# Kernel optimization log

Hardware: AMD Instinct MI355X
Metric: run time of the kernel (lower is better)

Reference implementation:

```python
import jax, jax.numpy as jnp
import numpy as np

NEG_SLOPE = 0.2


def gat_conv(x, src, dst, W, a_src, a_dst, b, heads, ch, n_nodes):
    # x: [N, F_in] -> h: [N, H, C]
    h = (x @ W).reshape(n_nodes, heads, ch)
    alpha_src = (h * a_src).sum(-1)  # [N, H]
    alpha_dst = (h * a_dst).sum(-1)  # [N, H]
    e = jax.nn.leaky_relu(alpha_src[src] + alpha_dst[dst], NEG_SLOPE)  # [E, H]
    # segment softmax over destination neighborhoods (every node has a self-loop)
    m = jax.ops.segment_max(e, dst, num_segments=n_nodes)
    e = jnp.exp(e - m[dst])
    s = jax.ops.segment_sum(e, dst, num_segments=n_nodes)
    alpha = e / s[dst]  # [E, H]
    out = jax.ops.segment_sum(h[src] * alpha[:, :, None], dst, num_segments=n_nodes)
    return out.reshape(n_nodes, heads * ch) + b


def setup_inputs() -> dict:
    key = jax.random.key(0)
    ks = jax.random.split(key, 12)
    N, E = 50000, 800000
    F_in, HID, H, OUT = 128, 64, 2, 64
    x = jax.random.normal(ks[0], (N, F_in), dtype=jnp.float32)
    edge_index = jax.random.randint(ks[1], (2, E), 0, N, dtype=jnp.int64)
    s1 = 1.0 / np.sqrt(F_in)
    s2 = 1.0 / np.sqrt(H * HID)
    return {
        "x": x,
        "edge_index": edge_index,
        "W1": jax.random.normal(ks[2], (F_in, H * HID), dtype=jnp.float32) * s1,
        "att_src1": jax.random.normal(ks[3], (H, HID), dtype=jnp.float32) * s1,
        "att_dst1": jax.random.normal(ks[4], (H, HID), dtype=jnp.float32) * s1,
        "b1": jnp.zeros((H * HID,), dtype=jnp.float32),
        "W2": jax.random.normal(ks[5], (H * HID, OUT), dtype=jnp.float32) * s2,
        "att_src2": jax.random.normal(ks[6], (1, OUT), dtype=jnp.float32) * s2,
        "att_dst2": jax.random.normal(ks[7], (1, OUT), dtype=jnp.float32) * s2,
        "b2": jnp.zeros((OUT,), dtype=jnp.float32),
    }


def reference(x, edge_index, W1, att_src1, att_dst1, b1, W2, att_src2, att_dst2, b2):
    N = x.shape[0]
    # PyG GATConv adds self-loops by default
    loops = jnp.arange(N, dtype=edge_index.dtype)
    src = jnp.concatenate([edge_index[0], loops])
    dst = jnp.concatenate([edge_index[1], loops])
    h = gat_conv(x, src, dst, W1, att_src1, att_dst1, b1, 2, 64, N)
    h = jax.nn.relu(h)
    out = gat_conv(h, src, dst, W2, att_src2, att_dst2, b2, 1, 64, N)
    return jax.nn.sigmoid(out)
```

## Files before the change

kernel.cpp:

```cpp
#include <hip/hip_runtime.h>
#include <math.h>

#define N_NODES 50000
#define N_EDGES 800000
#define E_TOT   (N_EDGES + N_NODES)
#define NEG_SLOPE 0.2f
#define NB_BKT  ((N_NODES + 255) / 256)
#define BKT_CAP 5632
#define P1_CHUNK 4096
#define NB_P1   ((E_TOT + P1_CHUNK - 1) / P1_CHUNK)
#define NB_G1   ((N_NODES + 127) / 128)

typedef short bf16x8 __attribute__((ext_vector_type(8)));
typedef float f32x4 __attribute__((ext_vector_type(4)));

static __device__ __forceinline__ float lrelu(float v) {
    return v > 0.0f ? v : NEG_SLOPE * v;
}

static __device__ __forceinline__ unsigned short f2bf(float f) {
    unsigned b = __float_as_uint(f);
    return (unsigned short)((b + 0x7fffu + ((b >> 16) & 1u)) >> 16);
}

static __device__ __forceinline__ float bflo(unsigned u) { return __uint_as_float(u << 16); }
static __device__ __forceinline__ float bfhi(unsigned u) { return __uint_as_float(u & 0xffff0000u); }

static __device__ __forceinline__ int swz(int row, int k) {
    return row * 128 + ((((k >> 3) ^ (row & 15)) << 3) | (k & 7));
}
static __device__ __forceinline__ int swz64(int row, int c) {
    return row * 64 + ((((c >> 3) ^ (row & 7)) << 3) | (c & 7));
}

__global__ __launch_bounds__(256, 2) void fusedA_kernel(const float* __restrict__ x,
                                                        const float* __restrict__ W,
                                                        const float* __restrict__ a_src,
                                                        const float* __restrict__ a_dst,
                                                        unsigned short* __restrict__ h1b,
                                                        float* __restrict__ as_out,
                                                        float* __restrict__ ad_out,
                                                        const int* __restrict__ ei,
                                                        int* __restrict__ bktcnt,
                                                        uint2* __restrict__ pairs) {
    __shared__ __align__(16) unsigned char smem[65536];
    int tid = threadIdx.x;

    if (blockIdx.x >= NB_G1) {
        int* cnt  = (int*)smem;
        int* base = (int*)(smem + 1024);
        for (int i = tid; i < NB_BKT; i += 256) cnt[i] = 0;
        __syncthreads();
        int cbase = (blockIdx.x - NB_G1) * P1_CHUNK;
        for (int i = tid; i < P1_CHUNK; i += 256) {
            int e = cbase + i;
            if (e >= E_TOT) break;
            int d = (e < N_EDGES) ? ei[N_EDGES + e] : (e - N_EDGES);
            atomicAdd(&cnt[d >> 8], 1);
        }
        __syncthreads();
        for (int i = tid; i < NB_BKT; i += 256) {
            int c = cnt[i];
            base[i] = c ? (BKT_CAP * i + atomicAdd(&bktcnt[i], c)) : 0;
            cnt[i] = 0;
        }
        __syncthreads();
        for (int i = tid; i < P1_CHUNK; i += 256) {
            int e = cbase + i;
            if (e >= E_TOT) break;
            int s, d;
            if (e < N_EDGES) { s = ei[e]; d = ei[N_EDGES + e]; }
            else { s = d = e - N_EDGES; }
            int bk = d >> 8;
            int p = base[bk] + atomicAdd(&cnt[bk], 1);
            pairs[p] = make_uint2((unsigned)s, (unsigned)d);
        }
        return;
    }

    unsigned short* xs = (unsigned short*)smem;
    unsigned short* wt = (unsigned short*)(smem + 32768);
    int r0 = blockIdx.x * 128;

    {
        int n = tid & 127;
        int c0 = (tid >> 7) * 8;
        for (int c = c0; c < c0 + 8; ++c) {
            int kb = c * 8;
            ushort4 lo, hi;
            lo.x = f2bf(W[(kb + 0) * 128 + n]);
            lo.y = f2bf(W[(kb + 1) * 128 + n]);
            lo.z = f2bf(W[(kb + 2) * 128 + n]);
            lo.w = f2bf(W[(kb + 3) * 128 + n]);
            hi.x = f2bf(W[(kb + 4) * 128 + n]);
            hi.y = f2bf(W[(kb + 5) * 128 + n]);
            hi.z = f2bf(W[(kb + 6) * 128 + n]);
            hi.w = f2bf(W[(kb + 7) * 128 + n]);
            int a = swz(n, kb);
            *(ushort4*)&wt[a] = lo;
            *(ushort4*)&wt[a + 4] = hi;
        }
    }
    {
        const int maxe = N_NODES * 128 - 4;
#pragma unroll
        for (int i = 0; i < 16384; i += 1024) {
            int e = i + tid * 4;
            int ge = r0 * 128 + e;
            if (ge > maxe) ge = maxe;
            float4 v = *(const float4*)&x[ge];
            ushort4 p;
            p.x = f2bf(v.x); p.y = f2bf(v.y); p.z = f2bf(v.z); p.w = f2bf(v.w);
            *(ushort4*)&xs[swz(e >> 7, e & 127)] = p;
        }
    }
    __syncthreads();

    int wv = tid >> 6, lane = tid & 63, lm = lane & 15, quad = lane >> 4;
    f32x4 acc[2][8];
#pragma unroll
    for (int m = 0; m < 2; ++m)
#pragma unroll
        for (int n = 0; n < 8; ++n) acc[m][n] = (f32x4){0.f, 0.f, 0.f, 0.f};

#pragma unroll
    for (int kc = 0; kc < 4; ++kc) {
        int kb = kc * 32 + quad * 8;
        bf16x8 a0 = *(bf16x8*)&xs[swz(wv * 32 + lm, kb)];
        bf16x8 a1 = *(bf16x8*)&xs[swz(wv * 32 + 16 + lm, kb)];
#pragma unroll
        for (int nt = 0; nt < 8; ++nt) {
            bf16x8 b = *(bf16x8*)&wt[swz(nt * 16 + lm, kb)];
            acc[0][nt] = __builtin_amdgcn_mfma_f32_16x16x32_bf16(a0, b, acc[0][nt], 0, 0, 0);
            acc[1][nt] = __builtin_amdgcn_mfma_f32_16x16x32_bf16(a1, b, acc[1][nt], 0, 0, 0);
        }
    }

    float asv[8], adv[8];
#pragma unroll
    for (int nt = 0; nt < 8; ++nt) {
        asv[nt] = a_src[nt * 16 + lm];
        adv[nt] = a_dst[nt * 16 + lm];
    }
#pragma unroll
    for (int mt = 0; mt < 2; ++mt) {
#pragma unroll
        for (int r = 0; r < 4; ++r) {
            float s0 = 0.f, s1 = 0.f, d0 = 0.f, d1 = 0.f;
#pragma unroll
            for (int nt = 0; nt < 4; ++nt) {
                s0 += acc[mt][nt][r] * asv[nt];
                d0 += acc[mt][nt][r] * adv[nt];
            }
#pragma unroll
            for (int nt = 4; nt < 8; ++nt) {
                s1 += acc[mt][nt][r] * asv[nt];
                d1 += acc[mt][nt][r] * adv[nt];
            }
#pragma unroll
            for (int m = 1; m < 16; m <<= 1) {
                s0 += __shfl_xor(s0, m, 64);
                s1 += __shfl_xor(s1, m, 64);
                d0 += __shfl_xor(d0, m, 64);
                d1 += __shfl_xor(d1, m, 64);
            }
            if (lm == 0) {
                int gr = r0 + wv * 32 + mt * 16 + quad * 4 + r;
                if (gr < N_NODES) {
                    as_out[gr * 2 + 0] = s0;
                    as_out[gr * 2 + 1] = s1;
                    ad_out[gr * 2 + 0] = d0;
                    ad_out[gr * 2 + 1] = d1;
                }
            }
        }
    }

    __syncthreads();
#pragma unroll
    for (int mt = 0; mt < 2; ++mt) {
#pragma unroll
        for (int nt = 0; nt < 8; ++nt) {
#pragma unroll
            for (int r = 0; r < 4; ++r) {
                int lrow = wv * 32 + mt * 16 + quad * 4 + r;
                xs[swz(lrow, nt * 16 + lm)] = f2bf(acc[mt][nt][r]);
            }
        }
    }
    __syncthreads();
    {
        int lrow = tid >> 1;
        int cb = (tid & 1) * 64;
        int gr = r0 + lrow;
        if (gr < N_NODES) {
            unsigned short* dst = h1b + (size_t)gr * 128 + cb;
#pragma unroll
            for (int c = 0; c < 8; ++c)
                *(uint4*)(dst + c * 8) = *(uint4*)&xs[swz(lrow, cb + c * 8)];
        }
    }
}

__global__ void scatterP2_kernel(const uint2* __restrict__ pairs, const int* __restrict__ bktcnt,
                                 int* __restrict__ offsets, int* __restrict__ deg,
                                 int* __restrict__ csr_src) {
    __shared__ int cnt[256];
    __shared__ int scn[256];
    int t = threadIdx.x;
    int b = blockIdx.x;
    int node0 = b << 8;
    int pbase = b * BKT_CAP;
    int cntE = bktcnt[b];
    cnt[t] = 0;
    __syncthreads();
    for (int j = t; j < cntE; j += 256)
        atomicAdd(&cnt[pairs[pbase + j].y - node0], 1);
    __syncthreads();
    int v = cnt[t];
    scn[t] = v;
    __syncthreads();
#pragma unroll
    for (int off = 1; off < 256; off <<= 1) {
        int u = (t >= off) ? scn[t - off] : 0;
        __syncthreads();
        scn[t] += u;
        __syncthreads();
    }
    int start = pbase + scn[t] - v;
    if (node0 + t < N_NODES) {
        offsets[node0 + t] = start;
        deg[node0 + t] = v;
    }
    cnt[t] = start;
    __syncthreads();
    for (int j = t; j < cntE; j += 256) {
        uint2 pr = pairs[pbase + j];
        int p = atomicAdd(&cnt[pr.y - node0], 1);
        csr_src[p] = (int)pr.x;
    }
}

__global__ __launch_bounds__(256, 2) void gemm2_kernel(const unsigned short* __restrict__ xb,
                                                       const float* __restrict__ W,
                                                       const float* __restrict__ a_src,
                                                       const float* __restrict__ a_dst,
                                                       unsigned short* __restrict__ h2b,
                                                       float* __restrict__ as_out,
                                                       float* __restrict__ ad_out) {
    __shared__ unsigned short xs[128 * 128];
    __shared__ unsigned short wt[64 * 128];
    int tid = threadIdx.x;
    int r0 = blockIdx.x * 128;

    {
        int n = tid & 63;
        int c0 = (tid >> 6) * 4;
        for (int c = c0; c < c0 + 4; ++c) {
            int kb = c * 8;
            ushort4 lo, hi;
            lo.x = f2bf(W[(kb + 0) * 64 + n]);
            lo.y = f2bf(W[(kb + 1) * 64 + n]);
            lo.z = f2bf(W[(kb + 2) * 64 + n]);
            lo.w = f2bf(W[(kb + 3) * 64 + n]);
            hi.x = f2bf(W[(kb + 4) * 64 + n]);
            hi.y = f2bf(W[(kb + 5) * 64 + n]);
            hi.z = f2bf(W[(kb + 6) * 64 + n]);
            hi.w = f2bf(W[(kb + 7) * 64 + n]);
            int a = swz(n, kb);
            *(ushort4*)&wt[a] = lo;
            *(ushort4*)&wt[a + 4] = hi;
        }
    }
    {
        const int maxe = N_NODES * 128 - 8;
#pragma unroll
        for (int i = 0; i < 16384; i += 2048) {
            int e = i + tid * 8;
            int ge = r0 * 128 + e;
            if (ge > maxe) ge = maxe;
            uint4 v = *(const uint4*)&xb[ge];
            *(uint4*)&xs[swz(e >> 7, e & 127)] = v;
        }
    }
    __syncthreads();

    int wv = tid >> 6, lane = tid & 63, lm = lane & 15, quad = lane >> 4;
    f32x4 acc[2][4];
#pragma unroll
    for (int m = 0; m < 2; ++m)
#pragma unroll
        for (int n = 0; n < 4; ++n) acc[m][n] = (f32x4){0.f, 0.f, 0.f, 0.f};

#pragma unroll
    for (int kc = 0; kc < 4; ++kc) {
        int kb = kc * 32 + quad * 8;
        bf16x8 a0 = *(bf16x8*)&xs[swz(wv * 32 + lm, kb)];
        bf16x8 a1 = *(bf16x8*)&xs[swz(wv * 32 + 16 + lm, kb)];
#pragma unroll
        for (int nt = 0; nt < 4; ++nt) {
            bf16x8 b = *(bf16x8*)&wt[swz(nt * 16 + lm, kb)];
            acc[0][nt] = __builtin_amdgcn_mfma_f32_16x16x32_bf16(a0, b, acc[0][nt], 0, 0, 0);
            acc[1][nt] = __builtin_amdgcn_mfma_f32_16x16x32_bf16(a1, b, acc[1][nt], 0, 0, 0);
        }
    }

    float asv[4], adv[4];
#pragma unroll
    for (int nt = 0; nt < 4; ++nt) {
        asv[nt] = a_src[nt * 16 + lm];
        adv[nt] = a_dst[nt * 16 + lm];
    }
#pragma unroll
    for (int mt = 0; mt < 2; ++mt) {
#pragma unroll
        for (int r = 0; r < 4; ++r) {
            float s0 = 0.f, d0 = 0.f;
#pragma unroll
            for (int nt = 0; nt < 4; ++nt) {
                s0 += acc[mt][nt][r] * asv[nt];
                d0 += acc[mt][nt][r] * adv[nt];
            }
#pragma unroll
            for (int m = 1; m < 16; m <<= 1) {
                s0 += __shfl_xor(s0, m, 64);
                d0 += __shfl_xor(d0, m, 64);
            }
            if (lm == 0) {
                int gr = r0 + wv * 32 + mt * 16 + quad * 4 + r;
                if (gr < N_NODES) {
                    as_out[gr] = s0;
                    ad_out[gr] = d0;
                }
            }
        }
    }

    __syncthreads();
#pragma unroll
    for (int mt = 0; mt < 2; ++mt) {
#pragma unroll
        for (int nt = 0; nt < 4; ++nt) {
#pragma unroll
            for (int r = 0; r < 4; ++r) {
                int lrow = wv * 32 + mt * 16 + quad * 4 + r;
                wt[swz64(lrow, nt * 16 + lm)] = f2bf(acc[mt][nt][r]);
            }
        }
    }
    __syncthreads();
    {
        int lrow = tid >> 1;
        int cb = (tid & 1) * 32;
        int gr = r0 + lrow;
        if (gr < N_NODES) {
            unsigned short* dst = h2b + (size_t)gr * 64 + cb;
#pragma unroll
            for (int c = 0; c < 4; ++c)
                *(uint4*)(dst + c * 8) = *(uint4*)&wt[swz64(lrow, cb + c * 8)];
        }
    }
}

__global__ void agg1_kernel(const unsigned short* __restrict__ h1b,
                            const float* __restrict__ as1,
                            const float* __restrict__ ad1, const float* __restrict__ b1,
                            const int* __restrict__ offsets, const int* __restrict__ deg,
                            const int* __restrict__ csr_src,
                            unsigned short* __restrict__ out1b) {
    int wid = (blockIdx.x * blockDim.x + threadIdx.x) >> 6;
    if (wid >= N_NODES) return;
    int lane = threadIdx.x & 63;
    int cl = lane & 31;
    int half = lane >> 5;
    bool head1 = (cl >= 16);
    float da0 = ad1[wid * 2 + 0], da1 = ad1[wid * 2 + 1];
    int jb = offsets[wid], je = jb + deg[wid];
    float a0 = 0.f, a1 = 0.f, a2 = 0.f, a3 = 0.f;
    float psum0 = 0.f, psum1 = 0.f;

    for (int chunk = jb; chunk < je; chunk += 64) {
        int j = chunk + lane;
        int s = 0; float w0 = 0.f, w1 = 0.f;
        if (j < je) {
            s = csr_src[j];
            float2 av = *(const float2*)&as1[s * 2];
            w0 = __expf(lrelu(av.x + da0));
            w1 = __expf(lrelu(av.y + da1));
        }
        psum0 += w0; psum1 += w1;
        int cnt = je - chunk; if (cnt > 64) cnt = 64;
        for (int k = 0; k < cnt; k += 8) {
            int k0 = k + half, k1 = k + 2 + half, k2 = k + 4 + half, k3 = k + 6 + half;
            int ss0 = __shfl(s, k0, 64);
            int ss1 = __shfl(s, k1, 64);
            int ss2 = __shfl(s, k2, 64);
            int ss3 = __shfl(s, k3, 64);
            uint2 u0 = ((const uint2*)(h1b + (size_t)ss0 * 128))[cl];
            uint2 u1 = ((const uint2*)(h1b + (size_t)ss1 * 128))[cl];
            uint2 u2 = ((const uint2*)(h1b + (size_t)ss2 * 128))[cl];
            uint2 u3 = ((const uint2*)(h1b + (size_t)ss3 * 128))[cl];
            float p0 = __shfl(w0, k0, 64), q0 = __shfl(w1, k0, 64);
            float p1 = __shfl(w0, k1, 64), q1 = __shfl(w1, k1, 64);
            float p2 = __shfl(w0, k2, 64), q2 = __shfl(w1, k2, 64);
            float p3 = __shfl(w0, k3, 64), q3 = __shfl(w1, k3, 64);
            float bw0 = head1 ? q0 : p0;
            float bw1 = head1 ? q1 : p1;
            float bw2 = head1 ? q2 : p2;
            float bw3 = head1 ? q3 : p3;
            a0 += bw0 * bflo(u0.x); a1 += bw0 * bfhi(u0.x); a2 += bw0 * bflo(u0.y); a3 += bw0 * bfhi(u0.y);
            a0 += bw1 * bflo(u1.x); a1 += bw1 * bfhi(u1.x); a2 += bw1 * bflo(u1.y); a3 += bw1 * bfhi(u1.y);
            a0 += bw2 * bflo(u2.x); a1 += bw2 * bfhi(u2.x); a2 += bw2 * bflo(u2.y); a3 += bw2 * bfhi(u2.y);
            a0 += bw3 * bflo(u3.x); a1 += bw3 * bfhi(u3.x); a2 += bw3 * bflo(u3.y); a3 += bw3 * bfhi(u3.y);
        }
    }
#pragma unroll
    for (int m = 1; m < 64; m <<= 1) {
        psum0 += __shfl_xor(psum0, m, 64);
        psum1 += __shfl_xor(psum1, m, 64);
    }
    float o0 = __shfl(a0, cl + 32, 64);
    float o1 = __shfl(a1, cl + 32, 64);
    float o2 = __shfl(a2, cl + 32, 64);
    float o3 = __shfl(a3, cl + 32, 64);
    if (lane < 32) {
        float inv = 1.f / (head1 ? psum1 : psum0);
        float4 bv = *(const float4*)&b1[cl * 4];
        float v0 = (a0 + o0) * inv + bv.x;
        float v1 = (a1 + o1) * inv + bv.y;
        float v2 = (a2 + o2) * inv + bv.z;
        float v3 = (a3 + o3) * inv + bv.w;
        v0 = v0 > 0.f ? v0 : 0.f;
        v1 = v1 > 0.f ? v1 : 0.f;
        v2 = v2 > 0.f ? v2 : 0.f;
        v3 = v3 > 0.f ? v3 : 0.f;
        ushort4 p;
        p.x = f2bf(v0); p.y = f2bf(v1); p.z = f2bf(v2); p.w = f2bf(v3);
        *(ushort4*)&out1b[(size_t)wid * 128 + cl * 4] = p;
    }
}

__global__ void agg2_kernel(const unsigned short* __restrict__ h2b,
                            const float* __restrict__ as2,
                            const float* __restrict__ ad2, const float* __restrict__ b2,
                            const int* __restrict__ offsets, const int* __restrict__ deg,
                            const int* __restrict__ csr_src,
                            float* __restrict__ out) {
    int wid = (blockIdx.x * blockDim.x + threadIdx.x) >> 6;
    if (wid >= N_NODES) return;
    int lane = threadIdx.x & 63;
    int cl = lane & 31;
    int half = lane >> 5;
    float da = ad2[wid];
    int jb = offsets[wid], je = jb + deg[wid];
    float acc0 = 0.f, acc1 = 0.f, psum = 0.f;

    for (int chunk = jb; chunk < je; chunk += 64) {
        int j = chunk + lane;
        int s = 0; float w = 0.f;
        if (j < je) {
            s = csr_src[j];
            w = __expf(lrelu(as2[s] + da));
        }
        psum += w;
        int cnt = je - chunk; if (cnt > 64) cnt = 64;
        for (int k = 0; k < cnt; k += 8) {
            int k0 = k + half, k1 = k + 2 + half, k2 = k + 4 + half, k3 = k + 6 + half;
            int ss0 = __shfl(s, k0, 64);
            int ss1 = __shfl(s, k1, 64);
            int ss2 = __shfl(s, k2, 64);
            int ss3 = __shfl(s, k3, 64);
            unsigned u0 = ((const unsigned*)(h2b + (size_t)ss0 * 64))[cl];
            unsigned u1 = ((const unsigned*)(h2b + (size_t)ss1 * 64))[cl];
            unsigned u2 = ((const unsigned*)(h2b + (size_t)ss2 * 64))[cl];
            unsigned u3 = ((const unsigned*)(h2b + (size_t)ss3 * 64))[cl];
            float bw0 = __shfl(w, k0, 64);
            float bw1 = __shfl(w, k1, 64);
            float bw2 = __shfl(w, k2, 64);
            float bw3 = __shfl(w, k3, 64);
            acc0 += bw0 * bflo(u0); acc1 += bw0 * bfhi(u0);
            acc0 += bw1 * bflo(u1); acc1 += bw1 * bfhi(u1);
            acc0 += bw2 * bflo(u2); acc1 += bw2 * bfhi(u2);
            acc0 += bw3 * bflo(u3); acc1 += bw3 * bfhi(u3);
        }
    }
#pragma unroll
    for (int m = 1; m < 64; m <<= 1) psum += __shfl_xor(psum, m, 64);
    float o0 = __shfl(acc0, cl + 32, 64);
    float o1 = __shfl(acc1, cl + 32, 64);
    if (lane < 32) {
        float inv = 1.f / psum;
        float2 bv = *(const float2*)&b2[cl * 2];
        float v0 = (acc0 + o0) * inv + bv.x;
        float v1 = (acc1 + o1) * inv + bv.y;
        v0 = 1.f / (1.f + __expf(-v0));
        v1 = 1.f / (1.f + __expf(-v1));
        *(float2*)&out[(size_t)wid * 64 + cl * 2] = make_float2(v0, v1);
    }
}

extern "C" void kernel_launch(void* const* d_in, const int* in_sizes, int n_in,
                              void* d_out, int out_size, void* d_ws, size_t ws_size,
                              hipStream_t stream) {
    const float* x     = (const float*)d_in[0];
    const int*   ei    = (const int*)d_in[1];
    const float* W1    = (const float*)d_in[2];
    const float* asrc1 = (const float*)d_in[3];
    const float* adst1 = (const float*)d_in[4];
    const float* b1    = (const float*)d_in[5];
    const float* W2    = (const float*)d_in[6];
    const float* asrc2 = (const float*)d_in[7];
    const float* adst2 = (const float*)d_in[8];
    const float* b2    = (const float*)d_in[9];
    float* out = (float*)d_out;

    float* ws = (float*)d_ws;
    size_t off = 0;
    float* as1  = ws + off; off += (size_t)N_NODES * 2;
    float* ad1  = ws + off; off += (size_t)N_NODES * 2;
    float* as2  = ws + off; off += (size_t)N_NODES;
    float* ad2  = ws + off; off += (size_t)N_NODES;
    unsigned short* h1b   = (unsigned short*)(ws + off); off += (size_t)N_NODES * 64;
    unsigned short* out1b = (unsigned short*)(ws + off); off += (size_t)N_NODES * 64;
    unsigned short* h2b   = (unsigned short*)(ws + off); off += (size_t)N_NODES * 32;
    int* offsets = (int*)(ws + off);
    int* deg     = offsets + N_NODES;
    int* csr_src = deg + N_NODES;
    int* bktcnt  = csr_src + NB_BKT * BKT_CAP;
    uint2* pairs = (uint2*)((((size_t)(bktcnt + NB_BKT)) + 7) & ~(size_t)7);

    hipMemsetAsync(bktcnt, 0, NB_BKT * sizeof(int), stream);

    fusedA_kernel<<<NB_G1 + NB_P1, 256, 0, stream>>>(x, W1, asrc1, adst1, h1b, as1, ad1,
                                                     ei, bktcnt, pairs);
    scatterP2_kernel<<<NB_BKT, 256, 0, stream>>>(pairs, bktcnt, offsets, deg, csr_src);
    agg1_kernel<<<(N_NODES * 64 + 255) / 256, 256, 0, stream>>>(h1b, as1, ad1, b1, offsets, deg, csr_src, out1b);
    gemm2_kernel<<<NB_G1, 256, 0, stream>>>(out1b, W2, asrc2, adst2, h2b, as2, ad2);
    agg2_kernel<<<(N_NODES * 64 + 255) / 256, 256, 0, stream>>>(h2b, as2, ad2, b2, offsets, deg, csr_src, out);
}
```

Baseline: 194.0 us.

## Fuse CSR scatter into layer-1 aggregation and store 16-bit source indices

Removes the separate scatter kernel: the layer-1 aggregation kernel now builds its bucket's CSR slice in shared memory and aggregates directly from it. Buckets shrink to 128 nodes and use 1024-thread blocks. Source indices are stored as unsigned short to halve index traffic in agg2. The cost is far fewer, larger blocks, which may reduce occupancy or balance in the gather-heavy aggregation.

```diff
diff --git a/kernel.cpp b/kernel.cpp
--- a/kernel.cpp
+++ b/kernel.cpp
@@ -5,8 +5,9 @@
 #define N_EDGES 800000
 #define E_TOT   (N_EDGES + N_NODES)
 #define NEG_SLOPE 0.2f
-#define NB_BKT  ((N_NODES + 255) / 256)
-#define BKT_CAP 5632
+#define NPB      128
+#define NB_BKT  ((N_NODES + NPB - 1) / NPB)
+#define BKT_CAP 3200
 #define P1_CHUNK 4096
 #define NB_P1   ((E_TOT + P1_CHUNK - 1) / P1_CHUNK)
 #define NB_G1   ((N_NODES + 127) / 128)
@@ -48,7 +49,7 @@
 
     if (blockIdx.x >= NB_G1) {
         int* cnt  = (int*)smem;
-        int* base = (int*)(smem + 1024);
+        int* base = (int*)(smem + 2048);
         for (int i = tid; i < NB_BKT; i += 256) cnt[i] = 0;
         __syncthreads();
         int cbase = (blockIdx.x - NB_G1) * P1_CHUNK;
@@ -56,7 +57,7 @@
             int e = cbase + i;
             if (e >= E_TOT) break;
             int d = (e < N_EDGES) ? ei[N_EDGES + e] : (e - N_EDGES);
-            atomicAdd(&cnt[d >> 8], 1);
+            atomicAdd(&cnt[d >> 7], 1);
         }
         __syncthreads();
         for (int i = tid; i < NB_BKT; i += 256) {
@@ -71,7 +72,7 @@
             int s, d;
             if (e < N_EDGES) { s = ei[e]; d = ei[N_EDGES + e]; }
             else { s = d = e - N_EDGES; }
-            int bk = d >> 8;
+            int bk = d >> 7;
             int p = base[bk] + atomicAdd(&cnt[bk], 1);
             pairs[p] = make_uint2((unsigned)s, (unsigned)d);
         }
@@ -202,42 +203,133 @@
     }
 }
 
-__global__ void scatterP2_kernel(const uint2* __restrict__ pairs, const int* __restrict__ bktcnt,
-                                 int* __restrict__ offsets, int* __restrict__ deg,
-                                 int* __restrict__ csr_src) {
-    __shared__ int cnt[256];
-    __shared__ int scn[256];
+__global__ __launch_bounds__(1024) void agg1_kernel(const unsigned short* __restrict__ h1b,
+                                                    const float* __restrict__ as1,
+                                                    const float* __restrict__ ad1,
+                                                    const float* __restrict__ b1,
+                                                    const uint2* __restrict__ pairs,
+                                                    const int* __restrict__ bktcnt,
+                                                    int* __restrict__ offsets,
+                                                    int* __restrict__ deg,
+                                                    unsigned short* __restrict__ csr_us,
+                                                    unsigned short* __restrict__ out1b) {
+    __shared__ unsigned short srcs[BKT_CAP];
+    __shared__ int cntL[NPB];
+    __shared__ int offL[NPB];
     int t = threadIdx.x;
     int b = blockIdx.x;
-    int node0 = b << 8;
+    int node0 = b * NPB;
     int pbase = b * BKT_CAP;
     int cntE = bktcnt[b];
-    cnt[t] = 0;
-    __syncthreads();
-    for (int j = t; j < cntE; j += 256)
-        atomicAdd(&cnt[pairs[pbase + j].y - node0], 1);
-    __syncthreads();
-    int v = cnt[t];
-    scn[t] = v;
-    __syncthreads();
-#pragma unroll
-    for (int off = 1; off < 256; off <<= 1) {
-        int u = (t >= off) ? scn[t - off] : 0;
+
+    if (t < NPB) cntL[t] = 0;
+    __syncthreads();
+    for (int j = t; j < cntE; j += 1024)
+        atomicAdd(&cntL[pairs[pbase + j].y - node0], 1);
+    __syncthreads();
+    int c = (t < NPB) ? cntL[t] : 0;
+    if (t < NPB) offL[t] = c;
+    __syncthreads();
+#pragma unroll
+    for (int off = 1; off < NPB; off <<= 1) {
+        int u = (t >= off && t < NPB) ? offL[t - off] : 0;
         __syncthreads();
-        scn[t] += u;
+        if (t < NPB) offL[t] += u;
         __syncthreads();
     }
-    int start = pbase + scn[t] - v;
-    if (node0 + t < N_NODES) {
-        offsets[node0 + t] = start;
-        deg[node0 + t] = v;
-    }
-    cnt[t] = start;
-    __syncthreads();
-    for (int j = t; j < cntE; j += 256) {
+    int excl = (t < NPB) ? (offL[t] - c) : 0;
+    if (t < NPB) {
+        int node = node0 + t;
+        if (node < N_NODES) {
+            offsets[node] = pbase + excl;
+            deg[node] = c;
+        }
+    }
+    __syncthreads();
+    if (t < NPB) { offL[t] = excl; cntL[t] = excl; }
+    __syncthreads();
+    for (int j = t; j < cntE; j += 1024) {
         uint2 pr = pairs[pbase + j];
-        int p = atomicAdd(&cnt[pr.y - node0], 1);
-        csr_src[p] = (int)pr.x;
+        int p = atomicAdd(&cntL[pr.y - node0], 1);
+        srcs[p] = (unsigned short)pr.x;
+    }
+    __syncthreads();
+    for (int j = t; j < cntE; j += 1024)
+        csr_us[pbase + j] = srcs[j];
+
+    int wv = t >> 6, lane = t & 63;
+    int cl = lane & 31;
+    int half = lane >> 5;
+    bool head1 = (cl >= 16);
+#pragma unroll
+    for (int nt = 0; nt < 8; ++nt) {
+        int nl = wv * 8 + nt;
+        int node = node0 + nl;
+        if (node >= N_NODES) continue;
+        int jb = offL[nl], je = cntL[nl];
+        float da0 = ad1[node * 2 + 0], da1 = ad1[node * 2 + 1];
+        float a0 = 0.f, a1 = 0.f, a2 = 0.f, a3 = 0.f;
+        float psum0 = 0.f, psum1 = 0.f;
+
+        for (int chunk = jb; chunk < je; chunk += 64) {
+            int j = chunk + lane;
+            int s = 0; float w0 = 0.f, w1 = 0.f;
+            if (j < je) {
+                s = (int)srcs[j];
+                float2 av = *(const float2*)&as1[s * 2];
+                w0 = __expf(lrelu(av.x + da0));
+                w1 = __expf(lrelu(av.y + da1));
+            }
+            psum0 += w0; psum1 += w1;
+            int cnt = je - chunk; if (cnt > 64) cnt = 64;
+            for (int k = 0; k < cnt; k += 8) {
+                int k0 = k + half, k1 = k + 2 + half, k2 = k + 4 + half, k3 = k + 6 + half;
+                int ss0 = __shfl(s, k0, 64);
+                int ss1 = __shfl(s, k1, 64);
+                int ss2 = __shfl(s, k2, 64);
+                int ss3 = __shfl(s, k3, 64);
+                uint2 u0 = ((const uint2*)(h1b + (size_t)ss0 * 128))[cl];
+                uint2 u1 = ((const uint2*)(h1b + (size_t)ss1 * 128))[cl];
+                uint2 u2 = ((const uint2*)(h1b + (size_t)ss2 * 128))[cl];
+                uint2 u3 = ((const uint2*)(h1b + (size_t)ss3 * 128))[cl];
+                float p0 = __shfl(w0, k0, 64), q0 = __shfl(w1, k0, 64);
+                float p1 = __shfl(w0, k1, 64), q1 = __shfl(w1, k1, 64);
+                float p2 = __shfl(w0, k2, 64), q2 = __shfl(w1, k2, 64);
+                float p3 = __shfl(w0, k3, 64), q3 = __shfl(w1, k3, 64);
+                float bw0 = head1 ? q0 : p0;
+                float bw1 = head1 ? q1 : p1;
+                float bw2 = head1 ? q2 : p2;
+                float bw3 = head1 ? q3 : p3;
+                a0 += bw0 * bflo(u0.x); a1 += bw0 * bfhi(u0.x); a2 += bw0 * bflo(u0.y); a3 += bw0 * bfhi(u0.y);
+                a0 += bw1 * bflo(u1.x); a1 += bw1 * bfhi(u1.x); a2 += bw1 * bflo(u1.y); a3 += bw1 * bfhi(u1.y);
+                a0 += bw2 * bflo(u2.x); a1 += bw2 * bfhi(u2.x); a2 += bw2 * bflo(u2.y); a3 += bw2 * bfhi(u2.y);
+                a0 += bw3 * bflo(u3.x); a1 += bw3 * bfhi(u3.x); a2 += bw3 * bflo(u3.y); a3 += bw3 * bfhi(u3.y);
+            }
+        }
+#pragma unroll
+        for (int m = 1; m < 64; m <<= 1) {
+            psum0 += __shfl_xor(psum0, m, 64);
+            psum1 += __shfl_xor(psum1, m, 64);
+        }
+        float o0 = __shfl(a0, cl + 32, 64);
+        float o1 = __shfl(a1, cl + 32, 64);
+        float o2 = __shfl(a2, cl + 32, 64);
+        float o3 = __shfl(a3, cl + 32, 64);
+        if (lane < 32) {
+            float inv = 1.f / (head1 ? psum1 : psum0);
+            float4 bv = *(const float4*)&b1[cl * 4];
+            float v0 = (a0 + o0) * inv + bv.x;
+            float v1 = (a1 + o1) * inv + bv.y;
+            float v2 = (a2 + o2) * inv + bv.z;
+            float v3 = (a3 + o3) * inv + bv.w;
+            v0 = v0 > 0.f ? v0 : 0.f;
+            v1 = v1 > 0.f ? v1 : 0.f;
+            v2 = v2 > 0.f ? v2 : 0.f;
+            v3 = v3 > 0.f ? v3 : 0.f;
+            ushort4 p;
+            p.x = f2bf(v0); p.y = f2bf(v1); p.z = f2bf(v2); p.w = f2bf(v3);
+            *(ushort4*)&out1b[(size_t)node * 128 + cl * 4] = p;
+        }
     }
 }
 
@@ -362,89 +454,11 @@
     }
 }
 
-__global__ void agg1_kernel(const unsigned short* __restrict__ h1b,
-                            const float* __restrict__ as1,
-                            const float* __restrict__ ad1, const float* __restrict__ b1,
-                            const int* __restrict__ offsets, const int* __restrict__ deg,
-                            const int* __restrict__ csr_src,
-                            unsigned short* __restrict__ out1b) {
-    int wid = (blockIdx.x * blockDim.x + threadIdx.x) >> 6;
-    if (wid >= N_NODES) return;
-    int lane = threadIdx.x & 63;
-    int cl = lane & 31;
-    int half = lane >> 5;
-    bool head1 = (cl >= 16);
-    float da0 = ad1[wid * 2 + 0], da1 = ad1[wid * 2 + 1];
-    int jb = offsets[wid], je = jb + deg[wid];
-    float a0 = 0.f, a1 = 0.f, a2 = 0.f, a3 = 0.f;
-    float psum0 = 0.f, psum1 = 0.f;
-
-    for (int chunk = jb; chunk < je; chunk += 64) {
-        int j = chunk + lane;
-        int s = 0; float w0 = 0.f, w1 = 0.f;
-        if (j < je) {
-            s = csr_src[j];
-            float2 av = *(const float2*)&as1[s * 2];
-            w0 = __expf(lrelu(av.x + da0));
-            w1 = __expf(lrelu(av.y + da1));
-        }
-        psum0 += w0; psum1 += w1;
-        int cnt = je - chunk; if (cnt > 64) cnt = 64;
-        for (int k = 0; k < cnt; k += 8) {
-            int k0 = k + half, k1 = k + 2 + half, k2 = k + 4 + half, k3 = k + 6 + half;
-            int ss0 = __shfl(s, k0, 64);
-            int ss1 = __shfl(s, k1, 64);
-            int ss2 = __shfl(s, k2, 64);
-            int ss3 = __shfl(s, k3, 64);
-            uint2 u0 = ((const uint2*)(h1b + (size_t)ss0 * 128))[cl];
-            uint2 u1 = ((const uint2*)(h1b + (size_t)ss1 * 128))[cl];
-            uint2 u2 = ((const uint2*)(h1b + (size_t)ss2 * 128))[cl];
-            uint2 u3 = ((const uint2*)(h1b + (size_t)ss3 * 128))[cl];
-            float p0 = __shfl(w0, k0, 64), q0 = __shfl(w1, k0, 64);
-            float p1 = __shfl(w0, k1, 64), q1 = __shfl(w1, k1, 64);
-            float p2 = __shfl(w0, k2, 64), q2 = __shfl(w1, k2, 64);
-            float p3 = __shfl(w0, k3, 64), q3 = __shfl(w1, k3, 64);
-            float bw0 = head1 ? q0 : p0;
-            float bw1 = head1 ? q1 : p1;
-            float bw2 = head1 ? q2 : p2;
-            float bw3 = head1 ? q3 : p3;
-            a0 += bw0 * bflo(u0.x); a1 += bw0 * bfhi(u0.x); a2 += bw0 * bflo(u0.y); a3 += bw0 * bfhi(u0.y);
-            a0 += bw1 * bflo(u1.x); a1 += bw1 * bfhi(u1.x); a2 += bw1 * bflo(u1.y); a3 += bw1 * bfhi(u1.y);
-            a0 += bw2 * bflo(u2.x); a1 += bw2 * bfhi(u2.x); a2 += bw2 * bflo(u2.y); a3 += bw2 * bfhi(u2.y);
-            a0 += bw3 * bflo(u3.x); a1 += bw3 * bfhi(u3.x); a2 += bw3 * bflo(u3.y); a3 += bw3 * bfhi(u3.y);
-        }
-    }
-#pragma unroll
-    for (int m = 1; m < 64; m <<= 1) {
-        psum0 += __shfl_xor(psum0, m, 64);
-        psum1 += __shfl_xor(psum1, m, 64);
-    }
-    float o0 = __shfl(a0, cl + 32, 64);
-    float o1 = __shfl(a1, cl + 32, 64);
-    float o2 = __shfl(a2, cl + 32, 64);
-    float o3 = __shfl(a3, cl + 32, 64);
-    if (lane < 32) {
-        float inv = 1.f / (head1 ? psum1 : psum0);
-        float4 bv = *(const float4*)&b1[cl * 4];
-        float v0 = (a0 + o0) * inv + bv.x;
-        float v1 = (a1 + o1) * inv + bv.y;
-        float v2 = (a2 + o2) * inv + bv.z;
-        float v3 = (a3 + o3) * inv + bv.w;
-        v0 = v0 > 0.f ? v0 : 0.f;
-        v1 = v1 > 0.f ? v1 : 0.f;
-        v2 = v2 > 0.f ? v2 : 0.f;
-        v3 = v3 > 0.f ? v3 : 0.f;
-        ushort4 p;
-        p.x = f2bf(v0); p.y = f2bf(v1); p.z = f2bf(v2); p.w = f2bf(v3);
-        *(ushort4*)&out1b[(size_t)wid * 128 + cl * 4] = p;
-    }
-}
-
 __global__ void agg2_kernel(const unsigned short* __restrict__ h2b,
                             const float* __restrict__ as2,
                             const float* __restrict__ ad2, const float* __restrict__ b2,
                             const int* __restrict__ offsets, const int* __restrict__ deg,
-                            const int* __restrict__ csr_src,
+                            const unsigned short* __restrict__ csr_us,
                             float* __restrict__ out) {
     int wid = (blockIdx.x * blockDim.x + threadIdx.x) >> 6;
     if (wid >= N_NODES) return;
@@ -459,7 +473,7 @@
         int j = chunk + lane;
         int s = 0; float w = 0.f;
         if (j < je) {
-            s = csr_src[j];
+            s = (int)csr_us[j];
             w = __expf(lrelu(as2[s] + da));
         }
         psum += w;
@@ -523,18 +537,19 @@
     unsigned short* h1b   = (unsigned short*)(ws + off); off += (size_t)N_NODES * 64;
     unsigned short* out1b = (unsigned short*)(ws + off); off += (size_t)N_NODES * 64;
     unsigned short* h2b   = (unsigned short*)(ws + off); off += (size_t)N_NODES * 32;
-    int* offsets = (int*)(ws + off);
-    int* deg     = offsets + N_NODES;
-    int* csr_src = deg + N_NODES;
-    int* bktcnt  = csr_src + NB_BKT * BKT_CAP;
-    uint2* pairs = (uint2*)((((size_t)(bktcnt + NB_BKT)) + 7) & ~(size_t)7);
+    int* offsets = (int*)(ws + off); off += N_NODES;
+    int* deg     = (int*)(ws + off); off += N_NODES;
+    unsigned short* csr_us = (unsigned short*)(ws + off);
+    off += ((size_t)NB_BKT * BKT_CAP + 1) / 2;
+    int* bktcnt  = (int*)(ws + off); off += NB_BKT;
+    uint2* pairs = (uint2*)((((size_t)(ws + off)) + 7) & ~(size_t)7);
 
     hipMemsetAsync(bktcnt, 0, NB_BKT * sizeof(int), stream);
 
     fusedA_kernel<<<NB_G1 + NB_P1, 256, 0, stream>>>(x, W1, asrc1, adst1, h1b, as1, ad1,
                                                      ei, bktcnt, pairs);
-    scatterP2_kernel<<<NB_BKT, 256, 0, stream>>>(pairs, bktcnt, offsets, deg, csr_src);
-    agg1_kernel<<<(N_NODES * 64 + 255) / 256, 256, 0, stream>>>(h1b, as1, ad1, b1, offsets, deg, csr_src, out1b);
+    agg1_kernel<<<NB_BKT, 1024, 0, stream>>>(h1b, as1, ad1, b1, pairs, bktcnt,
+                                             offsets, deg, csr_us, out1b);
     gemm2_kernel<<<NB_G1, 256, 0, stream>>>(out1b, W2, asrc2, adst2, h2b, as2, ad2);
-    agg2_kernel<<<(N_NODES * 64 + 255) / 256, 256, 0, stream>>>(h2b, as2, ad2, b2, offsets, deg, csr_src, out);
-}
+    agg2_kernel<<<(N_NODES * 64 + 255) / 256, 256, 0, stream>>>(h2b, as2, ad2, b2, offsets, deg, csr_us, out);
+}
```

New measurement: 196.9 us. Within noise of the previous version (+1.5%).
